# Optimization experiments

Measured on AMD Instinct MI355X. Metric: run time of the kernel, lower is better.

Reference implementation:

```python
import jax, jax.numpy as jnp
import numpy as np

B, S, H = 16, 1024, 64
HEADS, DH = 4, 16
EPS = 1e-5


def _layernorm(x, g, b):
    mu = jnp.mean(x, axis=-1, keepdims=True)
    var = jnp.mean(jnp.square(x - mu), axis=-1, keepdims=True)
    return (x - mu) * jax.lax.rsqrt(var + EPS) * g + b


def setup_inputs() -> dict:
    key = jax.random.key(0)
    ks = jax.random.split(key, 16)
    s = 1.0 / np.sqrt(H)
    inp = {
        'x': jax.random.normal(ks[0], (B, S, H), dtype=jnp.float32),
        'lengths': jax.random.randint(ks[1], (B,), 1, S + 1, dtype=jnp.int32),
        'atten': jnp.zeros((1,), dtype=jnp.float32),  # unused placeholder arg
        'Wq': jax.random.normal(ks[2], (H, H), dtype=jnp.float32) * s,
        'bq': jnp.zeros((H,), dtype=jnp.float32),
        'Wk': jax.random.normal(ks[3], (H, H), dtype=jnp.float32) * s,
        'bk': jnp.zeros((H,), dtype=jnp.float32),
        'Wv': jax.random.normal(ks[4], (H, H), dtype=jnp.float32) * s,
        'bv': jnp.zeros((H,), dtype=jnp.float32),
        'W1': jax.random.normal(ks[5], (H, H), dtype=jnp.float32) * s,
        'b1': jnp.zeros((H,), dtype=jnp.float32),
        'W2': jax.random.normal(ks[6], (H, H), dtype=jnp.float32) * s,
        'b2': jnp.zeros((H,), dtype=jnp.float32),
        'g1': jnp.ones((H,), dtype=jnp.float32),
        'be1': jnp.zeros((H,), dtype=jnp.float32),
        'g2': jnp.ones((H,), dtype=jnp.float32),
        'be2': jnp.zeros((H,), dtype=jnp.float32),
    }
    return inp


def reference(x, lengths, atten, Wq, bq, Wk, bk, Wv, bv, W1, b1, W2, b2, g1, be1, g2, be2):
    del atten  # overwritten in original forward before any use
    b, s, h = x.shape

    def proj(W, bias):
        p = x @ W.T + bias  # [b,s,h]
        return p.reshape(b, s, HEADS, DH).transpose(0, 2, 1, 3)  # [b,nh,s,dh]

    q, k, v = proj(Wq, bq), proj(Wk, bk), proj(Wv, bv)
    scores = jnp.einsum('bhqd,bhkd->bhqk', q, k) / np.float32(np.sqrt(h))

    causal = jnp.tril(jnp.ones((s, s), dtype=bool))  # [s,s]
    pos = jnp.arange(s)
    valid = pos[None, :] < lengths[:, None]  # [b,s]
    mask = causal[None, None] & valid[:, None, None, :] & valid[:, None, :, None]

    logits = jnp.where(mask, scores, jnp.float32(-1e30))
    att = jax.nn.softmax(logits, axis=-1) * mask  # zero fully-masked rows (NaN->0 trick)

    out = jnp.einsum('bhqk,bhkd->bhqd', att, v)
    out = out.transpose(0, 2, 1, 3).reshape(b, s, h)

    out_1 = x + out  # dropout is identity in eval mode
    out_1_norm = _layernorm(out_1, g1, be1)
    ff = jax.nn.gelu(out_1_norm @ W1.T + b1, approximate=False) @ W2.T + b2
    y_prim = _layernorm(out_1_norm + ff, g2, be2)

    atten_mean = jnp.mean(att, axis=1)  # [b,s,s], detached in original
    return (y_prim, atten_mean)
```

## Files before the change

### kernel.cpp

```cpp
#include <hip/hip_runtime.h>

#define NB 16
#define NS 1024
#define NHID 64
#define NHEADS 4
#define NDH 16
#define LN_EPS 1e-5f
#define QSCALE 0.18033688011112f

using v2h  = __attribute__((ext_vector_type(2))) _Float16;
using v4h  = __attribute__((ext_vector_type(4))) _Float16;
using v4f  = __attribute__((ext_vector_type(4))) float;

__device__ __forceinline__ v4h cvt4h(float4 a) {
    v4h r; r[0] = (_Float16)a.x; r[1] = (_Float16)a.y;
    r[2] = (_Float16)a.z; r[3] = (_Float16)a.w; return r;
}

__global__ __launch_bounds__(256) void qkv_mfma_kernel(
    const float* __restrict__ x,
    const float* __restrict__ Wq, const float* __restrict__ bq,
    const float* __restrict__ Wk, const float* __restrict__ bk,
    const float* __restrict__ Wv, const float* __restrict__ bv,
    _Float16* __restrict__ qh, _Float16* __restrict__ kh,
    _Float16* __restrict__ vt)
{
    const int t = threadIdx.x;
    const int w = t >> 6, l = t & 63;
    const int n16 = l & 15, g = l >> 4;
    const int rt = (int)blockIdx.x * 4 + w;
    const int srow0 = rt * 16;
    const int b = srow0 >> 10, s0 = srow0 & 1023;
    const size_t sg = (size_t)srow0 + n16;

    v4h xa[4];
    #pragma unroll
    for (int kb = 0; kb < 4; ++kb)
        xa[kb] = cvt4h(*(const float4*)&x[sg * 64 + kb * 16 + 4 * g]);

    #pragma unroll
    for (int m = 0; m < 3; ++m) {
        const float* W  = (m == 0) ? Wq : (m == 1) ? Wk : Wv;
        const float* bb = (m == 0) ? bq : (m == 1) ? bk : bv;
        #pragma unroll
        for (int mb = 0; mb < 4; ++mb) {
            const float4 bv4 = *(const float4*)&bb[mb * 16 + 4 * g];
            v4f acc = {bv4.x, bv4.y, bv4.z, bv4.w};
            #pragma unroll
            for (int kb = 0; kb < 4; ++kb) {
                v4h wf = cvt4h(*(const float4*)&W[(size_t)(mb * 16 + n16) * 64 + kb * 16 + 4 * g]);
                acc = __builtin_amdgcn_mfma_f32_16x16x16f16(wf, xa[kb], acc, 0, 0, 0);
            }
            const size_t hb = (size_t)(b * NHEADS + mb);
            if (m == 0) {
                v4h r = {(_Float16)(acc[0] * QSCALE), (_Float16)(acc[1] * QSCALE),
                         (_Float16)(acc[2] * QSCALE), (_Float16)(acc[3] * QSCALE)};
                *(v4h*)&qh[(hb * NS + s0 + n16) * NDH + 4 * g] = r;
            } else if (m == 1) {
                v4h r = {(_Float16)acc[0], (_Float16)acc[1], (_Float16)acc[2], (_Float16)acc[3]};
                *(v4h*)&kh[(hb * NS + s0 + n16) * NDH + 4 * g] = r;
            } else {
                #pragma unroll
                for (int i = 0; i < 4; ++i)
                    vt[(hb * NDH + 4 * g + i) * NS + s0 + n16] = (_Float16)acc[i];
            }
        }
    }
}

__global__ __launch_bounds__(1024, 8) void attn_ffn_kernel(
    const _Float16* __restrict__ qh, const _Float16* __restrict__ kh,
    const _Float16* __restrict__ vt, const int* __restrict__ lengths,
    const float* __restrict__ x,
    const float* __restrict__ W1, const float* __restrict__ b1,
    const float* __restrict__ W2, const float* __restrict__ b2,
    const float* __restrict__ g1, const float* __restrict__ be1,
    const float* __restrict__ g2, const float* __restrict__ be2,
    float* __restrict__ amean,
    float* __restrict__ y)
{
    __shared__ __align__(16) _Float16 Plds[2][2][NHEADS][16][72];
    __shared__ float zlds[4][NHEADS][16][2];
    __shared__ float aout_s[2][16][68];
    __shared__ __align__(16) _Float16 h1s[2][4][16][20];
    __shared__ float ln2s[2][4][16][2];

    const int t = threadIdx.x;
    const int wv = t >> 6;
    const int h  = wv & 3;
    const int kq = wv >> 2;
    const int l  = t & 63;
    const int g = l >> 4, n16 = l & 15;
    const int pr = blockIdx.x, b = blockIdx.y;
    const int len = lengths[b];
    const int q0A = pr << 4, q0B = (63 - pr) << 4;
    const int qA_ = q0A + n16, qB_ = q0B + n16;
    const bool qvA = qA_ < len, qvB = qB_ < len;
    const bool lenFA = len >= q0A + 16, lenFB = len >= q0B + 16;

    const size_t hbase = ((size_t)(b * NHEADS + h)) * NS;
    const v4h QA = *(const v4h*)&qh[(hbase + qA_) * NDH + 4 * g];
    const v4h QB = *(const v4h*)&qh[(hbase + qB_) * NDH + 4 * g];

    const int nkA = (len <= q0A) ? 0 : min(q0A + 16, len);
    const int nkB = (len <= q0B) ? 0 : min(q0B + 16, len);
    const int ntA = (nkA + 63) >> 6, ntB = (nkB + 63) >> 6;
    const int ntM = max(ntA, ntB);
    const v4f z4v = {0.f, 0.f, 0.f, 0.f};

    float ZA = 0.f, ZB = 0.f;
    for (int tile = 0; tile < ntM; ++tile) {
        const int ks = (tile << 6) + (kq << 4);
        const bool aA = ks < nkA, aB = ks < nkB;
        if (!aA && !aB) continue;
        const v4h K = *(const v4h*)&kh[(hbase + ks + n16) * NDH + 4 * g];
        if (aA) {
            v4f st = __builtin_amdgcn_mfma_f32_16x16x16f16(K, QA, z4v, 0, 0, 0);
            if (lenFA && (ks + 15 <= q0A)) {
                ZA += exp2f(st[0]) + exp2f(st[1]) + exp2f(st[2]) + exp2f(st[3]);
            } else {
                #pragma unroll
                for (int i = 0; i < 4; ++i) {
                    int kg = ks + 4 * g + i;
                    ZA += (qvA && kg <= qA_) ? exp2f(st[i]) : 0.f;
                }
            }
        }
        if (aB) {
            v4f st = __builtin_amdgcn_mfma_f32_16x16x16f16(K, QB, z4v, 0, 0, 0);
            if (lenFB && (ks + 15 <= q0B)) {
                ZB += exp2f(st[0]) + exp2f(st[1]) + exp2f(st[2]) + exp2f(st[3]);
            } else {
                #pragma unroll
                for (int i = 0; i < 4; ++i) {
                    int kg = ks + 4 * g + i;
                    ZB += (qvB && kg <= qB_) ? exp2f(st[i]) : 0.f;
                }
            }
        }
    }
    ZA += __shfl_xor(ZA, 16, 64); ZA += __shfl_xor(ZA, 32, 64);
    ZB += __shfl_xor(ZB, 16, 64); ZB += __shfl_xor(ZB, 32, 64);
    if (l < 16) {
        zlds[kq][h][n16][0] = ZA;
        zlds[kq][h][n16][1] = ZB;
    }
    __syncthreads();
    const float ztA = zlds[0][h][n16][0] + zlds[1][h][n16][0]
                    + zlds[2][h][n16][0] + zlds[3][h][n16][0];
    const float ztB = zlds[0][h][n16][1] + zlds[1][h][n16][1]
                    + zlds[2][h][n16][1] + zlds[3][h][n16][1];
    const float izA = (ztA > 0.f) ? 1.f / ztA : 0.f;
    const float izB = (ztB > 0.f) ? 1.f / ztB : 0.f;

    v4f oA = z4v, oB = z4v;
    const int pc = (kq << 4) + 4 * g;
    for (int tile = 0; tile < ntM; ++tile) {
        const int k0 = tile << 6;
        const int ks = k0 + (kq << 4);
        const int par = tile & 1;
        const bool aA = ks < nkA, aB = ks < nkB;
        v4h phA = {(_Float16)0.f, (_Float16)0.f, (_Float16)0.f, (_Float16)0.f};
        v4h phB = phA;
        if (aA || aB) {
            const v4h K = *(const v4h*)&kh[(hbase + ks + n16) * NDH + 4 * g];
            const v4h V = *(const v4h*)&vt[(((size_t)(b * NHEADS + h)) * NDH + n16) * NS + ks + 4 * g];
            if (aA) {
                v4f st = __builtin_amdgcn_mfma_f32_16x16x16f16(K, QA, z4v, 0, 0, 0);
                float p0, p1, p2, p3;
                if (lenFA && (ks + 15 <= q0A)) {
                    p0 = exp2f(st[0]) * izA; p1 = exp2f(st[1]) * izA;
                    p2 = exp2f(st[2]) * izA; p3 = exp2f(st[3]) * izA;
                } else {
                    const int kg = ks + 4 * g;
                    p0 = (qvA && kg + 0 <= qA_) ? exp2f(st[0]) * izA : 0.f;
                    p1 = (qvA && kg + 1 <= qA_) ? exp2f(st[1]) * izA : 0.f;
                    p2 = (qvA && kg + 2 <= qA_) ? exp2f(st[2]) * izA : 0.f;
                    p3 = (qvA && kg + 3 <= qA_) ? exp2f(st[3]) * izA : 0.f;
                }
                phA[0] = (_Float16)p0; phA[1] = (_Float16)p1;
                phA[2] = (_Float16)p2; phA[3] = (_Float16)p3;
                oA = __builtin_amdgcn_mfma_f32_16x16x16f16(phA, V, oA, 0, 0, 0);
            }
            if (aB) {
                v4f st = __builtin_amdgcn_mfma_f32_16x16x16f16(K, QB, z4v, 0, 0, 0);
                float p0, p1, p2, p3;
                if (lenFB && (ks + 15 <= q0B)) {
                    p0 = exp2f(st[0]) * izB; p1 = exp2f(st[1]) * izB;
                    p2 = exp2f(st[2]) * izB; p3 = exp2f(st[3]) * izB;
                } else {
                    const int kg = ks + 4 * g;
                    p0 = (qvB && kg + 0 <= qB_) ? exp2f(st[0]) * izB : 0.f;
                    p1 = (qvB && kg + 1 <= qB_) ? exp2f(st[1]) * izB : 0.f;
                    p2 = (qvB && kg + 2 <= qB_) ? exp2f(st[2]) * izB : 0.f;
                    p3 = (qvB && kg + 3 <= qB_) ? exp2f(st[3]) * izB : 0.f;
                }
                phB[0] = (_Float16)p0; phB[1] = (_Float16)p1;
                phB[2] = (_Float16)p2; phB[3] = (_Float16)p3;
                oB = __builtin_amdgcn_mfma_f32_16x16x16f16(phB, V, oB, 0, 0, 0);
            }
        }
        *(v4h*)&Plds[par][0][h][n16][pc] = phA;
        *(v4h*)&Plds[par][1][h][n16][pc] = phB;
        __syncthreads();
        {
            const int sid = t >> 9, r = (t >> 5) & 15, c2 = (t & 31) * 2;
            const bool go = (sid == 0) ? (tile < ntA) : (tile < ntB);
            if (go) {
                float s0 = 0.f, s1 = 0.f;
                #pragma unroll
                for (int hh = 0; hh < 4; ++hh) {
                    v2h pv = *(const v2h*)&Plds[par][sid][hh][r][c2];
                    s0 += (float)pv[0]; s1 += (float)pv[1];
                }
                const int q0 = sid ? q0B : q0A;
                float2 wv2 = make_float2(0.25f * s0, 0.25f * s1);
                *(float2*)&amean[((size_t)(b * NS + q0 + r)) * NS + k0 + c2] = wv2;
            }
        }
    }
    __syncthreads();

    float* obuf = (float*)Plds;
    {
        float* p = &obuf[(wv * 64 + l) * 8];
        p[0] = oA[0]; p[1] = oA[1]; p[2] = oA[2]; p[3] = oA[3];
        p[4] = oB[0]; p[5] = oB[1]; p[6] = oB[2]; p[7] = oB[3];
    }
    __syncthreads();
    if (kq == 0) {
        #pragma unroll
        for (int kq2 = 1; kq2 < 4; ++kq2) {
            const float* p = &obuf[(((h + 4 * kq2) * 64) + l) * 8];
            oA[0] += p[0]; oA[1] += p[1]; oA[2] += p[2]; oA[3] += p[3];
            oB[0] += p[4]; oB[1] += p[5]; oB[2] += p[6]; oB[3] += p[7];
        }
        #pragma unroll
        for (int i = 0; i < 4; ++i) {
            aout_s[0][4 * g + i][h * 16 + n16] = oA[i];
            aout_s[1][4 * g + i][h * 16 + n16] = oB[i];
        }
    }
    __syncthreads();

    const int side = wv >> 3;
    const int fw   = wv & 7;
    const bool fact = fw < 4;
    const int q0s  = side ? q0B : q0A;
    const size_t row = (size_t)(b * NS + q0s) + n16;

    float4 n1v[4]; v4h n1h[4];
    if (fact) {
        float4 o1f[4];
        #pragma unroll
        for (int kb = 0; kb < 4; ++kb) {
            float4 xv = *(const float4*)&x[row * 64 + kb * 16 + 4 * g];
            float4 av = *(const float4*)&aout_s[side][n16][kb * 16 + 4 * g];
            o1f[kb] = make_float4(xv.x + av.x, xv.y + av.y, xv.z + av.z, xv.w + av.w);
        }
        float s = 0.f;
        #pragma unroll
        for (int kb = 0; kb < 4; ++kb) s += o1f[kb].x + o1f[kb].y + o1f[kb].z + o1f[kb].w;
        s += __shfl_xor(s, 16, 64); s += __shfl_xor(s, 32, 64);
        const float mu = s * (1.f / 64.f);
        float vs = 0.f;
        #pragma unroll
        for (int kb = 0; kb < 4; ++kb) {
            float a = o1f[kb].x - mu, bb = o1f[kb].y - mu, c = o1f[kb].z - mu, d = o1f[kb].w - mu;
            vs += a * a + bb * bb + c * c + d * d;
        }
        vs += __shfl_xor(vs, 16, 64); vs += __shfl_xor(vs, 32, 64);
        const float rs = rsqrtf(vs * (1.f / 64.f) + LN_EPS);
        #pragma unroll
        for (int kb = 0; kb < 4; ++kb) {
            float4 gv  = *(const float4*)&g1[kb * 16 + 4 * g];
            float4 bev = *(const float4*)&be1[kb * 16 + 4 * g];
            n1v[kb].x = (o1f[kb].x - mu) * rs * gv.x + bev.x;
            n1v[kb].y = (o1f[kb].y - mu) * rs * gv.y + bev.y;
            n1v[kb].z = (o1f[kb].z - mu) * rs * gv.z + bev.z;
            n1v[kb].w = (o1f[kb].w - mu) * rs * gv.w + bev.w;
            n1h[kb] = cvt4h(n1v[kb]);
        }
        const float4 b1v = *(const float4*)&b1[fw * 16 + 4 * g];
        v4f acc = {b1v.x, b1v.y, b1v.z, b1v.w};
        #pragma unroll
        for (int kb = 0; kb < 4; ++kb) {
            v4h wf = cvt4h(*(const float4*)&W1[(size_t)(fw * 16 + n16) * 64 + kb * 16 + 4 * g]);
            acc = __builtin_amdgcn_mfma_f32_16x16x16f16(wf, n1h[kb], acc, 0, 0, 0);
        }
        v4h hh;
        #pragma unroll
        for (int i = 0; i < 4; ++i) {
            float a = acc[i];
            hh[i] = (_Float16)(0.5f * a * (1.f + erff(a * 0.70710678118654752f)));
        }
        *(v4h*)&h1s[side][fw][n16][4 * g] = hh;
    } else {
        const int nt = side ? ntB : ntA;
        const int kz = nt << 6;
        const int nz4 = (NS - kz) >> 2;
        const float4 zf = make_float4(0.f, 0.f, 0.f, 0.f);
        const int tt = (fw - 4) * 64 + l;
        for (int r = 0; r < 16; ++r)
            for (int c4 = tt; c4 < nz4; c4 += 256)
                *(float4*)&amean[((size_t)(b * NS + q0s + r)) * NS + kz + c4 * 4] = zf;
    }
    __syncthreads();

    float4 zrow;
    if (fact) {
        const float4 b2v = *(const float4*)&b2[fw * 16 + 4 * g];
        v4f acc = {b2v.x, b2v.y, b2v.z, b2v.w};
        #pragma unroll
        for (int db = 0; db < 4; ++db) {
            v4h hf = *(const v4h*)&h1s[side][db][n16][4 * g];
            v4h wf = cvt4h(*(const float4*)&W2[(size_t)(fw * 16 + n16) * 64 + db * 16 + 4 * g]);
            acc = __builtin_amdgcn_mfma_f32_16x16x16f16(wf, hf, acc, 0, 0, 0);
        }
        zrow = make_float4(n1v[fw].x + acc[0], n1v[fw].y + acc[1],
                           n1v[fw].z + acc[2], n1v[fw].w + acc[3]);
        float s2 = zrow.x + zrow.y + zrow.z + zrow.w;
        float q2 = zrow.x * zrow.x + zrow.y * zrow.y + zrow.z * zrow.z + zrow.w * zrow.w;
        s2 += __shfl_xor(s2, 16, 64); s2 += __shfl_xor(s2, 32, 64);
        q2 += __shfl_xor(q2, 16, 64); q2 += __shfl_xor(q2, 32, 64);
        if (g == 0) { ln2s[side][fw][n16][0] = s2; ln2s[side][fw][n16][1] = q2; }
    }
    __syncthreads();
    if (fact) {
        const float ts = ln2s[side][0][n16][0] + ln2s[side][1][n16][0]
                       + ln2s[side][2][n16][0] + ln2s[side][3][n16][0];
        const float tq = ln2s[side][0][n16][1] + ln2s[side][1][n16][1]
                       + ln2s[side][2][n16][1] + ln2s[side][3][n16][1];
        const float mu2 = ts * (1.f / 64.f);
        const float var2 = tq * (1.f / 64.f) - mu2 * mu2;
        const float rs2 = rsqrtf(var2 + LN_EPS);
        float4 gv  = *(const float4*)&g2[fw * 16 + 4 * g];
        float4 bev = *(const float4*)&be2[fw * 16 + 4 * g];
        float4 yv;
        yv.x = (zrow.x - mu2) * rs2 * gv.x + bev.x;
        yv.y = (zrow.y - mu2) * rs2 * gv.y + bev.y;
        yv.z = (zrow.z - mu2) * rs2 * gv.z + bev.z;
        yv.w = (zrow.w - mu2) * rs2 * gv.w + bev.w;
        *(float4*)&y[row * 64 + fw * 16 + 4 * g] = yv;
    }
}

extern "C" void kernel_launch(void* const* d_in, const int* in_sizes, int n_in,
                              void* d_out, int out_size, void* d_ws, size_t ws_size,
                              hipStream_t stream) {
    const float* x   = (const float*)d_in[0];
    const int* lengths = (const int*)d_in[1];
    const float* Wq  = (const float*)d_in[3];
    const float* bq  = (const float*)d_in[4];
    const float* Wk  = (const float*)d_in[5];
    const float* bk  = (const float*)d_in[6];
    const float* Wv  = (const float*)d_in[7];
    const float* bv  = (const float*)d_in[8];
    const float* W1  = (const float*)d_in[9];
    const float* b1  = (const float*)d_in[10];
    const float* W2  = (const float*)d_in[11];
    const float* b2  = (const float*)d_in[12];
    const float* g1  = (const float*)d_in[13];
    const float* be1 = (const float*)d_in[14];
    const float* g2  = (const float*)d_in[15];
    const float* be2 = (const float*)d_in[16];

    float* y     = (float*)d_out;
    float* amean = y + (size_t)NB * NS * NHID;

    const size_t nqkv = (size_t)NB * NHEADS * NS * NDH;
    _Float16* qhw = (_Float16*)d_ws;
    _Float16* khw = qhw + nqkv;
    _Float16* vtw = khw + nqkv;

    hipLaunchKernelGGL(qkv_mfma_kernel, dim3(NB * NS / 64), dim3(256), 0, stream,
                       x, Wq, bq, Wk, bk, Wv, bv, qhw, khw, vtw);
    hipLaunchKernelGGL(attn_ffn_kernel, dim3(32, NB), dim3(1024), 0, stream,
                       qhw, khw, vtw, lengths, x,
                       W1, b1, W2, b2, g1, be1, g2, be2,
                       amean, y);
}
```

Before: 63.27 us.

## Process one query tile per block instead of paired causal tiles

The attention+FFN kernel now handles a single 16-row query tile per workgroup, launched in reverse order (longest tiles first), with grid doubled to 64x16. The previous design paired tile p with tile 63-p so each block had balanced causal work; the new one removes the dual A/B paths, halves shared memory and register use, and lets 12 of 16 waves zero-fill amean instead of 4. It relies on hardware scheduling of heavy-first blocks for load balance, and doubles the block count, adding per-block overhead such as the FFN weight loads.

```diff
diff --git a/kernel.cpp b/kernel.cpp
--- a/kernel.cpp
+++ b/kernel.cpp
@@ -79,11 +79,11 @@
     float* __restrict__ amean,
     float* __restrict__ y)
 {
-    __shared__ __align__(16) _Float16 Plds[2][2][NHEADS][16][72];
-    __shared__ float zlds[4][NHEADS][16][2];
-    __shared__ float aout_s[2][16][68];
-    __shared__ __align__(16) _Float16 h1s[2][4][16][20];
-    __shared__ float ln2s[2][4][16][2];
+    __shared__ __align__(16) _Float16 Plds[2][NHEADS][16][72];
+    __shared__ float zlds[4][NHEADS][16];
+    __shared__ float aout_s[16][68];
+    __shared__ __align__(16) _Float16 h1s[4][16][20];
+    __shared__ float ln2s[4][16][2];
 
     const int t = threadIdx.x;
     const int wv = t >> 6;
@@ -91,171 +91,111 @@
     const int kq = wv >> 2;
     const int l  = t & 63;
     const int g = l >> 4, n16 = l & 15;
-    const int pr = blockIdx.x, b = blockIdx.y;
+    const int qt = 63 - (int)blockIdx.x;
+    const int b  = blockIdx.y;
     const int len = lengths[b];
-    const int q0A = pr << 4, q0B = (63 - pr) << 4;
-    const int qA_ = q0A + n16, qB_ = q0B + n16;
-    const bool qvA = qA_ < len, qvB = qB_ < len;
-    const bool lenFA = len >= q0A + 16, lenFB = len >= q0B + 16;
+    const int q0 = qt << 4;
+    const int qA_ = q0 + n16;
+    const bool qvA = qA_ < len;
+    const bool lenFA = len >= q0 + 16;
 
     const size_t hbase = ((size_t)(b * NHEADS + h)) * NS;
     const v4h QA = *(const v4h*)&qh[(hbase + qA_) * NDH + 4 * g];
-    const v4h QB = *(const v4h*)&qh[(hbase + qB_) * NDH + 4 * g];
-
-    const int nkA = (len <= q0A) ? 0 : min(q0A + 16, len);
-    const int nkB = (len <= q0B) ? 0 : min(q0B + 16, len);
-    const int ntA = (nkA + 63) >> 6, ntB = (nkB + 63) >> 6;
-    const int ntM = max(ntA, ntB);
+
+    const int nkA = (len <= q0) ? 0 : min(q0 + 16, len);
+    const int ntA = (nkA + 63) >> 6;
     const v4f z4v = {0.f, 0.f, 0.f, 0.f};
 
-    float ZA = 0.f, ZB = 0.f;
-    for (int tile = 0; tile < ntM; ++tile) {
+    float ZA = 0.f;
+    for (int tile = 0; tile < ntA; ++tile) {
         const int ks = (tile << 6) + (kq << 4);
-        const bool aA = ks < nkA, aB = ks < nkB;
-        if (!aA && !aB) continue;
+        if (ks >= nkA) continue;
         const v4h K = *(const v4h*)&kh[(hbase + ks + n16) * NDH + 4 * g];
-        if (aA) {
-            v4f st = __builtin_amdgcn_mfma_f32_16x16x16f16(K, QA, z4v, 0, 0, 0);
-            if (lenFA && (ks + 15 <= q0A)) {
-                ZA += exp2f(st[0]) + exp2f(st[1]) + exp2f(st[2]) + exp2f(st[3]);
-            } else {
-                #pragma unroll
-                for (int i = 0; i < 4; ++i) {
-                    int kg = ks + 4 * g + i;
-                    ZA += (qvA && kg <= qA_) ? exp2f(st[i]) : 0.f;
-                }
+        v4f st = __builtin_amdgcn_mfma_f32_16x16x16f16(K, QA, z4v, 0, 0, 0);
+        if (lenFA && (ks + 15 <= q0)) {
+            ZA += exp2f(st[0]) + exp2f(st[1]) + exp2f(st[2]) + exp2f(st[3]);
+        } else {
+            #pragma unroll
+            for (int i = 0; i < 4; ++i) {
+                int kg = ks + 4 * g + i;
+                ZA += (qvA && kg <= qA_) ? exp2f(st[i]) : 0.f;
             }
         }
-        if (aB) {
-            v4f st = __builtin_amdgcn_mfma_f32_16x16x16f16(K, QB, z4v, 0, 0, 0);
-            if (lenFB && (ks + 15 <= q0B)) {
-                ZB += exp2f(st[0]) + exp2f(st[1]) + exp2f(st[2]) + exp2f(st[3]);
-            } else {
-                #pragma unroll
-                for (int i = 0; i < 4; ++i) {
-                    int kg = ks + 4 * g + i;
-                    ZB += (qvB && kg <= qB_) ? exp2f(st[i]) : 0.f;
-                }
-            }
-        }
     }
     ZA += __shfl_xor(ZA, 16, 64); ZA += __shfl_xor(ZA, 32, 64);
-    ZB += __shfl_xor(ZB, 16, 64); ZB += __shfl_xor(ZB, 32, 64);
-    if (l < 16) {
-        zlds[kq][h][n16][0] = ZA;
-        zlds[kq][h][n16][1] = ZB;
-    }
-    __syncthreads();
-    const float ztA = zlds[0][h][n16][0] + zlds[1][h][n16][0]
-                    + zlds[2][h][n16][0] + zlds[3][h][n16][0];
-    const float ztB = zlds[0][h][n16][1] + zlds[1][h][n16][1]
-                    + zlds[2][h][n16][1] + zlds[3][h][n16][1];
+    if (l < 16) zlds[kq][h][n16] = ZA;
+    __syncthreads();
+    const float ztA = zlds[0][h][n16] + zlds[1][h][n16]
+                    + zlds[2][h][n16] + zlds[3][h][n16];
     const float izA = (ztA > 0.f) ? 1.f / ztA : 0.f;
-    const float izB = (ztB > 0.f) ? 1.f / ztB : 0.f;
-
-    v4f oA = z4v, oB = z4v;
+
+    v4f oA = z4v;
     const int pc = (kq << 4) + 4 * g;
-    for (int tile = 0; tile < ntM; ++tile) {
+    for (int tile = 0; tile < ntA; ++tile) {
         const int k0 = tile << 6;
         const int ks = k0 + (kq << 4);
         const int par = tile & 1;
-        const bool aA = ks < nkA, aB = ks < nkB;
         v4h phA = {(_Float16)0.f, (_Float16)0.f, (_Float16)0.f, (_Float16)0.f};
-        v4h phB = phA;
-        if (aA || aB) {
+        if (ks < nkA) {
             const v4h K = *(const v4h*)&kh[(hbase + ks + n16) * NDH + 4 * g];
             const v4h V = *(const v4h*)&vt[(((size_t)(b * NHEADS + h)) * NDH + n16) * NS + ks + 4 * g];
-            if (aA) {
-                v4f st = __builtin_amdgcn_mfma_f32_16x16x16f16(K, QA, z4v, 0, 0, 0);
-                float p0, p1, p2, p3;
-                if (lenFA && (ks + 15 <= q0A)) {
-                    p0 = exp2f(st[0]) * izA; p1 = exp2f(st[1]) * izA;
-                    p2 = exp2f(st[2]) * izA; p3 = exp2f(st[3]) * izA;
-                } else {
-                    const int kg = ks + 4 * g;
-                    p0 = (qvA && kg + 0 <= qA_) ? exp2f(st[0]) * izA : 0.f;
-                    p1 = (qvA && kg + 1 <= qA_) ? exp2f(st[1]) * izA : 0.f;
-                    p2 = (qvA && kg + 2 <= qA_) ? exp2f(st[2]) * izA : 0.f;
-                    p3 = (qvA && kg + 3 <= qA_) ? exp2f(st[3]) * izA : 0.f;
-                }
-                phA[0] = (_Float16)p0; phA[1] = (_Float16)p1;
-                phA[2] = (_Float16)p2; phA[3] = (_Float16)p3;
-                oA = __builtin_amdgcn_mfma_f32_16x16x16f16(phA, V, oA, 0, 0, 0);
+            v4f st = __builtin_amdgcn_mfma_f32_16x16x16f16(K, QA, z4v, 0, 0, 0);
+            float p0, p1, p2, p3;
+            if (lenFA && (ks + 15 <= q0)) {
+                p0 = exp2f(st[0]) * izA; p1 = exp2f(st[1]) * izA;
+                p2 = exp2f(st[2]) * izA; p3 = exp2f(st[3]) * izA;
+            } else {
+                const int kg = ks + 4 * g;
+                p0 = (qvA && kg + 0 <= qA_) ? exp2f(st[0]) * izA : 0.f;
+                p1 = (qvA && kg + 1 <= qA_) ? exp2f(st[1]) * izA : 0.f;
+                p2 = (qvA && kg + 2 <= qA_) ? exp2f(st[2]) * izA : 0.f;
+                p3 = (qvA && kg + 3 <= qA_) ? exp2f(st[3]) * izA : 0.f;
             }
-            if (aB) {
-                v4f st = __builtin_amdgcn_mfma_f32_16x16x16f16(K, QB, z4v, 0, 0, 0);
-                float p0, p1, p2, p3;
-                if (lenFB && (ks + 15 <= q0B)) {
-                    p0 = exp2f(st[0]) * izB; p1 = exp2f(st[1]) * izB;
-                    p2 = exp2f(st[2]) * izB; p3 = exp2f(st[3]) * izB;
-                } else {
-                    const int kg = ks + 4 * g;
-                    p0 = (qvB && kg + 0 <= qB_) ? exp2f(st[0]) * izB : 0.f;
-                    p1 = (qvB && kg + 1 <= qB_) ? exp2f(st[1]) * izB : 0.f;
-                    p2 = (qvB && kg + 2 <= qB_) ? exp2f(st[2]) * izB : 0.f;
-                    p3 = (qvB && kg + 3 <= qB_) ? exp2f(st[3]) * izB : 0.f;
-                }
-                phB[0] = (_Float16)p0; phB[1] = (_Float16)p1;
-                phB[2] = (_Float16)p2; phB[3] = (_Float16)p3;
-                oB = __builtin_amdgcn_mfma_f32_16x16x16f16(phB, V, oB, 0, 0, 0);
-            }
-        }
-        *(v4h*)&Plds[par][0][h][n16][pc] = phA;
-        *(v4h*)&Plds[par][1][h][n16][pc] = phB;
+            phA[0] = (_Float16)p0; phA[1] = (_Float16)p1;
+            phA[2] = (_Float16)p2; phA[3] = (_Float16)p3;
+            oA = __builtin_amdgcn_mfma_f32_16x16x16f16(phA, V, oA, 0, 0, 0);
+        }
+        *(v4h*)&Plds[par][h][n16][pc] = phA;
         __syncthreads();
         {
-            const int sid = t >> 9, r = (t >> 5) & 15, c2 = (t & 31) * 2;
-            const bool go = (sid == 0) ? (tile < ntA) : (tile < ntB);
-            if (go) {
-                float s0 = 0.f, s1 = 0.f;
-                #pragma unroll
-                for (int hh = 0; hh < 4; ++hh) {
-                    v2h pv = *(const v2h*)&Plds[par][sid][hh][r][c2];
-                    s0 += (float)pv[0]; s1 += (float)pv[1];
-                }
-                const int q0 = sid ? q0B : q0A;
-                float2 wv2 = make_float2(0.25f * s0, 0.25f * s1);
-                *(float2*)&amean[((size_t)(b * NS + q0 + r)) * NS + k0 + c2] = wv2;
-            }
+            const int r = t >> 6, c = t & 63;
+            float s = (float)Plds[par][0][r][c] + (float)Plds[par][1][r][c]
+                    + (float)Plds[par][2][r][c] + (float)Plds[par][3][r][c];
+            amean[((size_t)(b * NS + q0 + r)) * NS + k0 + c] = 0.25f * s;
         }
     }
     __syncthreads();
 
     float* obuf = (float*)Plds;
     {
-        float* p = &obuf[(wv * 64 + l) * 8];
+        float* p = &obuf[(wv * 64 + l) * 4];
         p[0] = oA[0]; p[1] = oA[1]; p[2] = oA[2]; p[3] = oA[3];
-        p[4] = oB[0]; p[5] = oB[1]; p[6] = oB[2]; p[7] = oB[3];
     }
     __syncthreads();
     if (kq == 0) {
         #pragma unroll
         for (int kq2 = 1; kq2 < 4; ++kq2) {
-            const float* p = &obuf[(((h + 4 * kq2) * 64) + l) * 8];
+            const float* p = &obuf[(((h + 4 * kq2) * 64) + l) * 4];
             oA[0] += p[0]; oA[1] += p[1]; oA[2] += p[2]; oA[3] += p[3];
-            oB[0] += p[4]; oB[1] += p[5]; oB[2] += p[6]; oB[3] += p[7];
-        }
-        #pragma unroll
-        for (int i = 0; i < 4; ++i) {
-            aout_s[0][4 * g + i][h * 16 + n16] = oA[i];
-            aout_s[1][4 * g + i][h * 16 + n16] = oB[i];
-        }
-    }
-    __syncthreads();
-
-    const int side = wv >> 3;
-    const int fw   = wv & 7;
-    const bool fact = fw < 4;
-    const int q0s  = side ? q0B : q0A;
-    const size_t row = (size_t)(b * NS + q0s) + n16;
-
-    float4 n1v[4]; v4h n1h[4];
+        }
+        #pragma unroll
+        for (int i = 0; i < 4; ++i)
+            aout_s[4 * g + i][h * 16 + n16] = oA[i];
+    }
+    __syncthreads();
+
+    const bool fact = wv < 4;
+    const int fw = wv;
+    const size_t row = (size_t)(b * NS + q0) + n16;
+
+    v4h n1h[4];
+    float4 n1self;
     if (fact) {
         float4 o1f[4];
         #pragma unroll
         for (int kb = 0; kb < 4; ++kb) {
             float4 xv = *(const float4*)&x[row * 64 + kb * 16 + 4 * g];
-            float4 av = *(const float4*)&aout_s[side][n16][kb * 16 + 4 * g];
+            float4 av = *(const float4*)&aout_s[n16][kb * 16 + 4 * g];
             o1f[kb] = make_float4(xv.x + av.x, xv.y + av.y, xv.z + av.z, xv.w + av.w);
         }
         float s = 0.f;
@@ -275,11 +215,13 @@
         for (int kb = 0; kb < 4; ++kb) {
             float4 gv  = *(const float4*)&g1[kb * 16 + 4 * g];
             float4 bev = *(const float4*)&be1[kb * 16 + 4 * g];
-            n1v[kb].x = (o1f[kb].x - mu) * rs * gv.x + bev.x;
-            n1v[kb].y = (o1f[kb].y - mu) * rs * gv.y + bev.y;
-            n1v[kb].z = (o1f[kb].z - mu) * rs * gv.z + bev.z;
-            n1v[kb].w = (o1f[kb].w - mu) * rs * gv.w + bev.w;
-            n1h[kb] = cvt4h(n1v[kb]);
+            float4 nv;
+            nv.x = (o1f[kb].x - mu) * rs * gv.x + bev.x;
+            nv.y = (o1f[kb].y - mu) * rs * gv.y + bev.y;
+            nv.z = (o1f[kb].z - mu) * rs * gv.z + bev.z;
+            nv.w = (o1f[kb].w - mu) * rs * gv.w + bev.w;
+            n1h[kb] = cvt4h(nv);
+            if (kb == fw) n1self = nv;
         }
         const float4 b1v = *(const float4*)&b1[fw * 16 + 4 * g];
         v4f acc = {b1v.x, b1v.y, b1v.z, b1v.w};
@@ -294,16 +236,15 @@
             float a = acc[i];
             hh[i] = (_Float16)(0.5f * a * (1.f + erff(a * 0.70710678118654752f)));
         }
-        *(v4h*)&h1s[side][fw][n16][4 * g] = hh;
+        *(v4h*)&h1s[fw][n16][4 * g] = hh;
     } else {
-        const int nt = side ? ntB : ntA;
-        const int kz = nt << 6;
+        const int kz = ntA << 6;
         const int nz4 = (NS - kz) >> 2;
         const float4 zf = make_float4(0.f, 0.f, 0.f, 0.f);
-        const int tt = (fw - 4) * 64 + l;
+        const int tt = (wv - 4) * 64 + l;
         for (int r = 0; r < 16; ++r)
-            for (int c4 = tt; c4 < nz4; c4 += 256)
-                *(float4*)&amean[((size_t)(b * NS + q0s + r)) * NS + kz + c4 * 4] = zf;
+            for (int c4 = tt; c4 < nz4; c4 += 768)
+                *(float4*)&amean[((size_t)(b * NS + q0 + r)) * NS + kz + c4 * 4] = zf;
     }
     __syncthreads();
 
@@ -313,24 +254,24 @@
         v4f acc = {b2v.x, b2v.y, b2v.z, b2v.w};
         #pragma unroll
         for (int db = 0; db < 4; ++db) {
-            v4h hf = *(const v4h*)&h1s[side][db][n16][4 * g];
+            v4h hf = *(const v4h*)&h1s[db][n16][4 * g];
             v4h wf = cvt4h(*(const float4*)&W2[(size_t)(fw * 16 + n16) * 64 + db * 16 + 4 * g]);
             acc = __builtin_amdgcn_mfma_f32_16x16x16f16(wf, hf, acc, 0, 0, 0);
         }
-        zrow = make_float4(n1v[fw].x + acc[0], n1v[fw].y + acc[1],
-                           n1v[fw].z + acc[2], n1v[fw].w + acc[3]);
+        zrow = make_float4(n1self.x + acc[0], n1self.y + acc[1],
+                           n1self.z + acc[2], n1self.w + acc[3]);
         float s2 = zrow.x + zrow.y + zrow.z + zrow.w;
         float q2 = zrow.x * zrow.x + zrow.y * zrow.y + zrow.z * zrow.z + zrow.w * zrow.w;
         s2 += __shfl_xor(s2, 16, 64); s2 += __shfl_xor(s2, 32, 64);
         q2 += __shfl_xor(q2, 16, 64); q2 += __shfl_xor(q2, 32, 64);
-        if (g == 0) { ln2s[side][fw][n16][0] = s2; ln2s[side][fw][n16][1] = q2; }
+        if (g == 0) { ln2s[fw][n16][0] = s2; ln2s[fw][n16][1] = q2; }
     }
     __syncthreads();
     if (fact) {
-        const float ts = ln2s[side][0][n16][0] + ln2s[side][1][n16][0]
-                       + ln2s[side][2][n16][0] + ln2s[side][3][n16][0];
-        const float tq = ln2s[side][0][n16][1] + ln2s[side][1][n16][1]
-                       + ln2s[side][2][n16][1] + ln2s[side][3][n16][1];
+        const float ts = ln2s[0][n16][0] + ln2s[1][n16][0]
+                       + ln2s[2][n16][0] + ln2s[3][n16][0];
+        const float tq = ln2s[0][n16][1] + ln2s[1][n16][1]
+                       + ln2s[2][n16][1] + ln2s[3][n16][1];
         const float mu2 = ts * (1.f / 64.f);
         const float var2 = tq * (1.f / 64.f) - mu2 * mu2;
         const float rs2 = rsqrtf(var2 + LN_EPS);
@@ -375,7 +316,7 @@
 
     hipLaunchKernelGGL(qkv_mfma_kernel, dim3(NB * NS / 64), dim3(256), 0, stream,
                        x, Wq, bq, Wk, bk, Wv, bv, qhw, khw, vtw);
-    hipLaunchKernelGGL(attn_ffn_kernel, dim3(32, NB), dim3(1024), 0, stream,
+    hipLaunchKernelGGL(attn_ffn_kernel, dim3(64, NB), dim3(1024), 0, stream,
                        qhw, khw, vtw, lengths, x,
                        W1, b1, W2, b2, g1, be1, g2, be2,
                        amean, y);
```

Result: faster. 60.90 us (-3.8%).
